# Optimization experiments

Measured on AMD Instinct MI355X. Metric: run time of the kernel, lower is better.

The kernel has to match this reference:

```python
import jax, jax.numpy as jnp
import numpy as np

B, S, D, H, E, K = 1, 2048, 1024, 16, 8, 2
DK = D // H          # 64 per-head key dim
FF = 4 * D           # 4096 expert hidden
EPS = 1e-5


def rmsnorm(x, scale):
    rms = jnp.sqrt(jnp.mean(x * x, axis=-1, keepdims=True) + EPS)
    return scale * (x / rms)


def setup_inputs() -> dict:
    key = jax.random.key(0)
    ks = jax.random.split(key, 12)
    std = 0.02
    x = jax.random.normal(ks[0], (B, S, D), dtype=jnp.float32)
    # causal mask: masked_fill where mask == 0
    self_attn_mask = jnp.tril(jnp.ones((S, S), dtype=jnp.int32))
    scale_attn = jnp.ones((D,), dtype=jnp.float32)
    scale_ffn = jnp.ones((D,), dtype=jnp.float32)
    # per-head projections, stacked: [H, DK, D] (torch Linear weight layout [out,in])
    Wq = jax.random.normal(ks[1], (H, DK, D), dtype=jnp.float32) * std
    Wk = jax.random.normal(ks[2], (H, DK, D), dtype=jnp.float32) * std
    Wv = jax.random.normal(ks[3], (H, DK, D), dtype=jnp.float32) * std
    Wo = jax.random.normal(ks[4], (D, D), dtype=jnp.float32) * std
    Wg = jax.random.normal(ks[5], (E, D), dtype=jnp.float32) * std   # router gate
    W_in = jax.random.normal(ks[6], (E, FF, D), dtype=jnp.float32) * std   # expert linear
    W_v = jax.random.normal(ks[7], (E, FF, D), dtype=jnp.float32) * std    # expert linear_v
    W_out = jax.random.normal(ks[8], (E, D, FF), dtype=jnp.float32) * std  # expert linear_out
    return {
        'x': x, 'self_attn_mask': self_attn_mask,
        'scale_attn': scale_attn, 'Wq': Wq, 'Wk': Wk, 'Wv': Wv, 'Wo': Wo,
        'scale_ffn': scale_ffn, 'Wg': Wg, 'W_in': W_in, 'W_v': W_v, 'W_out': W_out,
    }


def reference(x, self_attn_mask, scale_attn, Wq, Wk, Wv, Wo, scale_ffn, Wg, W_in, W_v, W_out):
    # --- self attention (pre-RMSNorm) ---
    normed = rmsnorm(x, scale_attn)
    q = jnp.einsum('bsd,hkd->bhsk', normed, Wq)
    k = jnp.einsum('bsd,hkd->bhsk', normed, Wk)
    v = jnp.einsum('bsd,hkd->bhsk', normed, Wv)
    attn = jnp.einsum('bhsk,bhtk->bhst', q, k) / np.sqrt(DK).astype(np.float32)
    attn = jnp.where(self_attn_mask[None, None] == 0, -jnp.inf, attn)
    attn = jax.nn.softmax(attn, axis=-1)
    ctx = jnp.einsum('bhst,bhtk->bhsk', attn, v)
    ctx = ctx.transpose(0, 2, 1, 3).reshape(x.shape[0], x.shape[1], D)  # concat heads
    a1 = ctx @ Wo.T
    x = x + a1
    # --- MoE (pre-RMSNorm) ---
    normed = rmsnorm(x, scale_ffn)
    router_logits = normed @ Wg.T                       # [B,S,E]
    router_probs = jax.nn.softmax(router_logits, axis=-1)
    gate, idx = jax.lax.top_k(router_probs, K)          # [B,S,K]
    gate = gate / jnp.sum(gate, axis=-1, keepdims=True)
    # combine weights per expert: sum of renormalized gates over selected slots
    onehot = (idx[..., None] == jnp.arange(E)).astype(x.dtype)  # [B,S,K,E]
    combine = jnp.sum(gate[..., None] * onehot, axis=2)         # [B,S,E]
    # all-expert dense FFN (faithful to the masked dense loop in torch)
    g = jax.nn.gelu(jnp.einsum('bsd,efd->bsef', normed, W_in), approximate=False)
    val = jnp.einsum('bsd,efd->bsef', normed, W_v)
    eo = jnp.einsum('bsef,edf->bsed', g * val, W_out)           # [B,S,E,D]
    moe_out = jnp.einsum('bse,bsed->bsd', combine, eo)
    out = x + moe_out
    return (out, router_probs)
```

## Files before the change

kernel.cpp:

```cpp
#include <hip/hip_runtime.h>
#include <hip/hip_bf16.h>
#include <math.h>

typedef unsigned int u32;
typedef unsigned short u16;
using bf16x8 = __attribute__((ext_vector_type(8))) short;
using f32x4 = __attribute__((ext_vector_type(4))) float;

#define MFMA_BF16(a, b, c) __builtin_amdgcn_mfma_f32_16x16x32_bf16((a), (b), (c), 0, 0, 0)
#define VMCNT8() asm volatile("s_waitcnt vmcnt(8)" ::: "memory")
#define VMCNT6() asm volatile("s_waitcnt vmcnt(6)" ::: "memory")
#define VMCNT4() asm volatile("s_waitcnt vmcnt(4)" ::: "memory")
#define VMCNT0() asm volatile("s_waitcnt vmcnt(0)" ::: "memory")
#define SBAR() __builtin_amdgcn_s_barrier()
#define SCHED0() __builtin_amdgcn_sched_barrier(0)

constexpr int kS = 2048, kD = 1024, kH = 16, kE = 8, kFF = 4096;
constexpr int kSlotCap = 5120;
constexpr int kMaxTiles = 40;
constexpr int kChunk = 8;

__device__ __forceinline__ u16 bf16_rne(float f) {
  u32 u = __float_as_uint(f);
  u32 r = (u + 0x7fffu + ((u >> 16) & 1u)) >> 16;
  return (u16)r;
}
__device__ __forceinline__ float bf16_f32(u16 h) { return __uint_as_float(((u32)h) << 16); }
__device__ __forceinline__ u32 pack_hl(float x) {
  u16 hi = bf16_rne(x);
  u16 lo = bf16_rne(x - bf16_f32(hi));
  return ((u32)lo << 16) | (u32)hi;
}
__device__ __forceinline__ void unpack8(const u32* t, bf16x8& h, bf16x8& l) {
#pragma unroll
  for (int j = 0; j < 8; j++) {
    h[j] = (short)(t[j] & 0xffffu);
    l[j] = (short)(t[j] >> 16);
  }
}
__device__ __forceinline__ void gload_lds16(const void* g, void* l) {
  __builtin_amdgcn_global_load_lds((const __attribute__((address_space(1))) u32*)g,
                                   (__attribute__((address_space(3))) u32*)l, 16, 0, 0);
}
__device__ __forceinline__ u32 cvtpk(float a, float b) {
  u32 r;
  asm("v_cvt_pk_bf16_f32 %0, %1, %2" : "=v"(r) : "v"(a), "v"(b));
  return r;
}

__global__ __launch_bounds__(256) void pack_dp3(const float* __restrict__ Wq,
                                                const float* __restrict__ Wk,
                                                const float* __restrict__ Wv,
                                                u16* __restrict__ o) {
  int i = blockIdx.x * 256 + threadIdx.x;
  if (i >= 3072 * 1024) return;
  int n = i >> 10, k = i & 1023;
  float v = (n < 1024) ? Wq[i] : (n < 2048) ? Wk[i - 1024 * 1024] : Wv[i - 2048 * 1024];
  u16 hi = bf16_rne(v);
  u16 lo = bf16_rne(v - bf16_f32(hi));
  size_t b = (size_t)n * 2048 + (size_t)(k >> 5) * 64 + (k & 31);
  o[b] = hi;
  o[b + 32] = lo;
}
__global__ __launch_bounds__(256) void pack_dp1(const float* __restrict__ W,
                                                u16* __restrict__ o, int n_elem) {
  int i = blockIdx.x * 256 + threadIdx.x;
  if (i >= n_elem) return;
  int k = i & 1023, n = i >> 10;
  float v = W[i];
  u16 hi = bf16_rne(v);
  u16 lo = bf16_rne(v - bf16_f32(hi));
  size_t b = (size_t)n * 2048 + (size_t)(k >> 5) * 64 + (k & 31);
  o[b] = hi;
  o[b + 32] = lo;
}
__global__ __launch_bounds__(256) void pack_bf16_kernel(const float* __restrict__ w,
                                                        u16* __restrict__ o, int n8) {
  int i = blockIdx.x * 256 + threadIdx.x;
  if (i >= n8) return;
  const float4* s = (const float4*)w + (size_t)i * 2;
  float4 a = s[0], b = s[1];
  u16 r[8] = {bf16_rne(a.x), bf16_rne(a.y), bf16_rne(a.z), bf16_rne(a.w),
              bf16_rne(b.x), bf16_rne(b.y), bf16_rne(b.z), bf16_rne(b.w)};
  *(uint4*)(o + (size_t)i * 8) = *(uint4*)r;
}

template <int MODE>
__global__ __launch_bounds__(256) void rmsnorm_kernel(
    const float* __restrict__ x, const float* __restrict__ scale,
    u16* __restrict__ odp, float* __restrict__ of32, u16* __restrict__ ob16) {
  const int s = blockIdx.x;
  const float* row = x + (size_t)s * kD;
  const int c = threadIdx.x * 4;
  float4 v = *(const float4*)(row + c);
  float ss = v.x * v.x + v.y * v.y + v.z * v.z + v.w * v.w;
#pragma unroll
  for (int m = 32; m; m >>= 1) ss += __shfl_xor(ss, m);
  __shared__ float wsum[4];
  if ((threadIdx.x & 63) == 0) wsum[threadIdx.x >> 6] = ss;
  __syncthreads();
  float tot = wsum[0] + wsum[1] + wsum[2] + wsum[3];
  float rinv = 1.0f / sqrtf(tot * (1.0f / kD) + 1e-5f);
  float4 sc = *(const float4*)(scale + c);
  float n[4] = {v.x * rinv * sc.x, v.y * rinv * sc.y, v.z * rinv * sc.z, v.w * rinv * sc.w};
  if (MODE == 0) {
    u16 hv[4], lv[4];
#pragma unroll
    for (int j = 0; j < 4; j++) {
      hv[j] = bf16_rne(n[j]);
      lv[j] = bf16_rne(n[j] - bf16_f32(hv[j]));
    }
    u16* o = odp + (size_t)s * 2048 + (size_t)(c >> 5) * 64 + (c & 31);
    *(uint2*)o = *(uint2*)hv;
    *(uint2*)(o + 32) = *(uint2*)lv;
  } else {
    *(float4*)(of32 + (size_t)s * kD + c) = make_float4(n[0], n[1], n[2], n[3]);
    u16* o = ob16 + (size_t)s * kD + c;
    o[0] = bf16_rne(n[0]); o[1] = bf16_rne(n[1]); o[2] = bf16_rne(n[2]); o[3] = bf16_rne(n[3]);
  }
}

template <int APK, int OUT>
__global__ __launch_bounds__(256) void gemm_dp(
    const void* __restrict__ Av, const u16* __restrict__ Bdp,
    const float* __restrict__ resid, int K,
    u32* __restrict__ oq, u32* __restrict__ ok, u32* __restrict__ ov,
    float* __restrict__ of) {
  __shared__ u16 As[2][128 * 64];
  __shared__ u16 Bs[2][128 * 64];
  const int tid = threadIdx.x, w = tid >> 6, l = tid & 63;
  const int m0 = blockIdx.y * 128, n0 = blockIdx.x * 128;
  const int wr = (w >> 1) * 64, wc = (w & 1) * 64;
  const char* Ab = (const char*)Av;
  const char* Bb = (const char*)Bdp;
  const size_t rowb = (size_t)K * 4;

  size_t asrc[4], bsrc[4];
  int dst[4];
#pragma unroll
  for (int i = 0; i < 4; i++) {
    int fl = i * 256 + tid;
    int row = fl >> 3, cb = fl & 7;
    size_t coff = (size_t)((cb ^ (row & 7)) * 16);
    asrc[i] = (size_t)(m0 + row) * rowb + coff;
    bsrc[i] = (size_t)(n0 + row) * rowb + coff;
    dst[i] = fl * 16;
  }

  f32x4 zero = {0.f, 0.f, 0.f, 0.f};
  f32x4 acc[4][4];
#pragma unroll
  for (int i = 0; i < 4; i++)
#pragma unroll
    for (int j = 0; j < 4; j++) acc[i][j] = zero;

  auto stage = [&](int buf, int s) {
    const char* ap = Ab + (size_t)s * 128;
    const char* bp = Bb + (size_t)s * 128;
#pragma unroll
    for (int i = 0; i < 4; i++) {
      gload_lds16(ap + asrc[i], (char*)&As[buf][0] + dst[i]);
      gload_lds16(bp + bsrc[i], (char*)&Bs[buf][0] + dst[i]);
    }
  };

  const int NS = K / 32;
  stage(0, 0);
  for (int s = 0; s < NS; s++) {
    const int cur = s & 1;
    const bool lastit = (s == NS - 1);
    if (!lastit) stage(cur ^ 1, s + 1);
    if (!lastit) VMCNT8(); else VMCNT0();
    SBAR();
    SCHED0();
    bf16x8 ah[4], al[4], bh[4], bl[4];
    const int g = l >> 4;
    if (APK) {
      const u32* At = (const u32*)&As[cur][0];
#pragma unroll
      for (int mi = 0; mi < 4; mi++) {
        int row = wr + mi * 16 + (l & 15);
        u32 t[8];
        *(uint4*)t = *(const uint4*)&At[row * 32 + (((2 * g) ^ (row & 7)) * 4)];
        *(uint4*)(t + 4) = *(const uint4*)&At[row * 32 + (((2 * g + 1) ^ (row & 7)) * 4)];
        unpack8(t, ah[mi], al[mi]);
      }
    } else {
#pragma unroll
      for (int mi = 0; mi < 4; mi++) {
        int row = wr + mi * 16 + (l & 15);
        ah[mi] = *(const bf16x8*)&As[cur][row * 64 + ((g ^ (row & 7)) * 8)];
        al[mi] = *(const bf16x8*)&As[cur][row * 64 + (((4 + g) ^ (row & 7)) * 8)];
      }
    }
#pragma unroll
    for (int ni = 0; ni < 4; ni++) {
      int row = wc + ni * 16 + (l & 15);
      bh[ni] = *(const bf16x8*)&Bs[cur][row * 64 + ((g ^ (row & 7)) * 8)];
      bl[ni] = *(const bf16x8*)&Bs[cur][row * 64 + (((4 + g) ^ (row & 7)) * 8)];
    }
#pragma unroll
    for (int mi = 0; mi < 4; mi++)
#pragma unroll
      for (int ni = 0; ni < 4; ni++) {
        f32x4 c = acc[mi][ni];
        c = MFMA_BF16(al[mi], bh[ni], c);
        c = MFMA_BF16(ah[mi], bl[ni], c);
        c = MFMA_BF16(ah[mi], bh[ni], c);
        acc[mi][ni] = c;
      }
    SCHED0();
    if (!lastit) SBAR();
  }

  if (OUT == 0) {
    u32* dstp;
    int nb;
    if (n0 < 1024) { dstp = oq; nb = n0; }
    else if (n0 < 2048) { dstp = ok; nb = n0 - 1024; }
    else { dstp = ov; nb = n0 - 2048; }
#pragma unroll
    for (int mi = 0; mi < 4; mi++)
#pragma unroll
      for (int ni = 0; ni < 4; ni++)
#pragma unroll
        for (int r = 0; r < 4; r++) {
          int row = m0 + wr + mi * 16 + ((l >> 4) << 2) + r;
          int col = nb + wc + ni * 16 + (l & 15);
          dstp[(size_t)row * 1024 + col] = pack_hl(acc[mi][ni][r]);
        }
  } else {
#pragma unroll
    for (int mi = 0; mi < 4; mi++)
#pragma unroll
      for (int ni = 0; ni < 4; ni++)
#pragma unroll
        for (int r = 0; r < 4; r++) {
          int row = m0 + wr + mi * 16 + ((l >> 4) << 2) + r;
          int col = n0 + wc + ni * 16 + (l & 15);
          of[(size_t)row * 1024 + col] = resid[(size_t)row * 1024 + col] + acc[mi][ni][r];
        }
  }
}

__global__ __launch_bounds__(256) void attn_kernel(
    const u32* __restrict__ Qp, const u32* __restrict__ Kp, const u32* __restrict__ Vp,
    float* __restrict__ Opart, float* __restrict__ mpart, float* __restrict__ lpart) {
  constexpr int LDK = 68;
  __shared__ u32 Ks[64 * LDK];
  __shared__ u32 Vs[64 * LDK];
  __shared__ u32 Ps[64 * LDK];
  const int tid = threadIdx.x, w = tid >> 6, l = tid & 63;
  int b = blockIdx.x, qt, c;
  if (b < 8) { qt = b; c = 0; }
  else if (b < 24) { qt = 8 + ((b - 8) >> 1); c = (b - 8) & 1; }
  else if (b < 48) { qt = 16 + (b - 24) / 3; c = (b - 24) % 3; }
  else { qt = 24 + ((b - 48) >> 2); c = (b - 48) & 3; }
  const int hh = blockIdx.y;
  const int q0 = qt * 64, hc = hh * 64;
  const int kt0 = c * kChunk;
  const int kt1 = min(kt0 + kChunk, qt + 1);

  bf16x8 qh[2], ql[2];
  {
    const int qrow = q0 + w * 16 + (l & 15);
#pragma unroll
    for (int kk = 0; kk < 2; kk++) {
      u32 t[8];
      const u32* p = Qp + (size_t)qrow * kD + hc + kk * 32 + ((l >> 4) << 3);
      *(uint4*)t = *(const uint4*)p;
      *(uint4*)(t + 4) = *(const uint4*)(p + 4);
      unpack8(t, qh[kk], ql[kk]);
    }
  }
  float mrun[4], lrun[4];
  f32x4 zero = {0.f, 0.f, 0.f, 0.f};
  f32x4 oacc[4];
#pragma unroll
  for (int r = 0; r < 4; r++) { mrun[r] = -3.0e38f; lrun[r] = 0.f; }
#pragma unroll
  for (int vb = 0; vb < 4; vb++) oacc[vb] = zero;

  const int trow = tid >> 2, c0v = (tid & 3) * 16;
  const u32* gKb = Kp + hc + c0v;
  const u32* gVb = Vp + hc + c0v;
  uint4 kr[4], vr[4];
  {
    const u32* gK = gKb + (size_t)(kt0 * 64 + trow) * kD;
    kr[0] = *(const uint4*)gK; kr[1] = *(const uint4*)(gK + 4);
    kr[2] = *(const uint4*)(gK + 8); kr[3] = *(const uint4*)(gK + 12);
    const u32* gV = gVb + (size_t)(kt0 * 64 + trow) * kD;
    vr[0] = *(const uint4*)gV; vr[1] = *(const uint4*)(gV + 4);
    vr[2] = *(const uint4*)(gV + 8); vr[3] = *(const uint4*)(gV + 12);
  }

  for (int kt = kt0; kt < kt1; kt++) {
    {
      u32* sK = Ks + trow * LDK + c0v;
      *(uint4*)sK = kr[0]; *(uint4*)(sK + 4) = kr[1];
      *(uint4*)(sK + 8) = kr[2]; *(uint4*)(sK + 12) = kr[3];
#pragma unroll
      for (int j = 0; j < 4; j++) {
        Vs[(c0v + j * 4 + 0) * LDK + trow] = vr[j].x;
        Vs[(c0v + j * 4 + 1) * LDK + trow] = vr[j].y;
        Vs[(c0v + j * 4 + 2) * LDK + trow] = vr[j].z;
        Vs[(c0v + j * 4 + 3) * LDK + trow] = vr[j].w;
      }
    }
    __syncthreads();
    if (kt + 1 < kt1) {
      const u32* gK = gKb + (size_t)((kt + 1) * 64 + trow) * kD;
      kr[0] = *(const uint4*)gK; kr[1] = *(const uint4*)(gK + 4);
      kr[2] = *(const uint4*)(gK + 8); kr[3] = *(const uint4*)(gK + 12);
      const u32* gV = gVb + (size_t)((kt + 1) * 64 + trow) * kD;
      vr[0] = *(const uint4*)gV; vr[1] = *(const uint4*)(gV + 4);
      vr[2] = *(const uint4*)(gV + 8); vr[3] = *(const uint4*)(gV + 12);
    }

    f32x4 sfr[4];
#pragma unroll
    for (int kb = 0; kb < 4; kb++) {
      f32x4 sa = zero;
#pragma unroll
      for (int kk = 0; kk < 2; kk++) {
        u32 t[8];
        bf16x8 kh, kl;
        const u32* p = Ks + (kb * 16 + (l & 15)) * LDK + kk * 32 + ((l >> 4) << 3);
        *(uint4*)t = *(const uint4*)p;
        *(uint4*)(t + 4) = *(const uint4*)(p + 4);
        unpack8(t, kh, kl);
        sa = MFMA_BF16(ql[kk], kl, sa);
        sa = MFMA_BF16(ql[kk], kh, sa);
        sa = MFMA_BF16(qh[kk], kl, sa);
        sa = MFMA_BF16(qh[kk], kh, sa);
      }
      sfr[kb] = sa * 0.125f;
    }
    if (kt == qt) {
#pragma unroll
      for (int kb = 0; kb < 4; kb++) {
        int t = kt * 64 + kb * 16 + (l & 15);
#pragma unroll
        for (int r = 0; r < 4; r++) {
          int qq = q0 + w * 16 + ((l >> 4) << 2) + r;
          if (t > qq) sfr[kb][r] = -3.0e38f;
        }
      }
    }
#pragma unroll
    for (int r = 0; r < 4; r++) {
      float mx = fmaxf(fmaxf(sfr[0][r], sfr[1][r]), fmaxf(sfr[2][r], sfr[3][r]));
#pragma unroll
      for (int mm = 1; mm < 16; mm <<= 1) mx = fmaxf(mx, __shfl_xor(mx, mm));
      float mnew = fmaxf(mrun[r], mx);
      float sf = __expf(mrun[r] - mnew);
      mrun[r] = mnew;
      float rs = 0.f;
#pragma unroll
      for (int kb = 0; kb < 4; kb++) {
        float p = __expf(sfr[kb][r] - mnew);
        sfr[kb][r] = p;
        rs += p;
      }
#pragma unroll
      for (int mm = 1; mm < 16; mm <<= 1) rs += __shfl_xor(rs, mm);
      lrun[r] = lrun[r] * sf + rs;
#pragma unroll
      for (int vb = 0; vb < 4; vb++) oacc[vb][r] *= sf;
    }
#pragma unroll
    for (int kb = 0; kb < 4; kb++)
#pragma unroll
      for (int r = 0; r < 4; r++)
        Ps[(w * 16 + ((l >> 4) << 2) + r) * LDK + kb * 16 + (l & 15)] = pack_hl(sfr[kb][r]);
#pragma unroll
    for (int ks = 0; ks < 2; ks++) {
      bf16x8 ph, pl;
      {
        u32 t[8];
        const u32* pp = Ps + (w * 16 + (l & 15)) * LDK + ks * 32 + ((l >> 4) << 3);
        *(uint4*)t = *(const uint4*)pp;
        *(uint4*)(t + 4) = *(const uint4*)(pp + 4);
        unpack8(t, ph, pl);
      }
#pragma unroll
      for (int vb = 0; vb < 4; vb++) {
        u32 t2[8];
        bf16x8 vh, vl;
        const u32* pv = Vs + (vb * 16 + (l & 15)) * LDK + ks * 32 + ((l >> 4) << 3);
        *(uint4*)t2 = *(const uint4*)pv;
        *(uint4*)(t2 + 4) = *(const uint4*)(pv + 4);
        unpack8(t2, vh, vl);
        f32x4 cc = oacc[vb];
        cc = MFMA_BF16(pl, vl, cc);
        cc = MFMA_BF16(pl, vh, cc);
        cc = MFMA_BF16(ph, vl, cc);
        cc = MFMA_BF16(ph, vh, cc);
        oacc[vb] = cc;
      }
    }
    __syncthreads();
  }

  const int p = (qt * 16 + hh) * 4 + c;
  float* Po = Opart + (size_t)p * 4096;
#pragma unroll
  for (int vb = 0; vb < 4; vb++)
#pragma unroll
    for (int r = 0; r < 4; r++) {
      int rl = w * 16 + ((l >> 4) << 2) + r;
      int cl = vb * 16 + (l & 15);
      Po[rl * 64 + cl] = oacc[vb][r];
    }
  if ((l & 15) == 0) {
#pragma unroll
    for (int r = 0; r < 4; r++) {
      int rl = w * 16 + ((l >> 4) << 2) + r;
      mpart[p * 64 + rl] = mrun[r];
      lpart[p * 64 + rl] = lrun[r];
    }
  }
}

__global__ __launch_bounds__(256) void attn_merge(
    const float* __restrict__ Opart, const float* __restrict__ mpart,
    const float* __restrict__ lpart, u32* __restrict__ Op) {
  const int qt = blockIdx.x, hh = blockIdx.y;
  const int nch = (qt + kChunk) >> 3;
  const int t = threadIdx.x;
  const int row = t >> 2;
  const int c0 = (t & 3) * 16;
  const int pbase = (qt * 16 + hh) * 4;
  float M = -3.0e38f;
  for (int c = 0; c < nch; c++) M = fmaxf(M, mpart[(pbase + c) * 64 + row]);
  float den = 0.f;
  float acc[16];
#pragma unroll
  for (int j = 0; j < 16; j++) acc[j] = 0.f;
  for (int c = 0; c < nch; c++) {
    float wgt = __expf(mpart[(pbase + c) * 64 + row] - M);
    den += wgt * lpart[(pbase + c) * 64 + row];
    const float* po = Opart + (size_t)(pbase + c) * 4096 + row * 64 + c0;
#pragma unroll
    for (int j = 0; j < 16; j += 4) {
      float4 v = *(const float4*)(po + j);
      acc[j] += wgt * v.x; acc[j + 1] += wgt * v.y;
      acc[j + 2] += wgt * v.z; acc[j + 3] += wgt * v.w;
    }
  }
  float inv = 1.f / den;
  u32* dst = Op + (size_t)(qt * 64 + row) * kD + hh * 64 + c0;
#pragma unroll
  for (int j = 0; j < 16; j++) dst[j] = pack_hl(acc[j] * inv);
}

__global__ __launch_bounds__(256) void router_kernel(
    const float* __restrict__ normed, const float* __restrict__ Wg,
    float* __restrict__ probs, float* __restrict__ gates,
    int* __restrict__ experts, int* __restrict__ counts) {
  const int w = threadIdx.x >> 6, l = threadIdx.x & 63;
  const int s = blockIdx.x * 4 + w;
  float lg[kE];
  const float* row = normed + (size_t)s * kD;
#pragma unroll
  for (int e = 0; e < kE; e++) {
    const float* wg = Wg + (size_t)e * kD;
    float a = 0.f;
    for (int d = l; d < kD; d += 64) a += row[d] * wg[d];
#pragma unroll
    for (int m = 32; m; m >>= 1) a += __shfl_xor(a, m);
    lg[e] = a;
  }
  if (l == 0) {
    float mx = lg[0];
#pragma unroll
    for (int e = 1; e < kE; e++) mx = fmaxf(mx, lg[e]);
    float p[kE], sum = 0.f;
#pragma unroll
    for (int e = 0; e < kE; e++) { p[e] = __expf(lg[e] - mx); sum += p[e]; }
    float inv = 1.f / sum;
#pragma unroll
    for (int e = 0; e < kE; e++) { p[e] *= inv; probs[(size_t)s * kE + e] = p[e]; }
    int i1 = 0;
#pragma unroll
    for (int e = 1; e < kE; e++) if (lg[e] > lg[i1]) i1 = e;
    int i2 = (i1 == 0) ? 1 : 0;
#pragma unroll
    for (int e = 0; e < kE; e++) if (e != i1 && lg[e] > lg[i2]) i2 = e;
    float den = 1.f / (p[i1] + p[i2]);
    gates[s * 2] = p[i1] * den;
    gates[s * 2 + 1] = p[i2] * den;
    experts[s * 2] = i1;
    experts[s * 2 + 1] = i2;
    atomicAdd(&counts[i1], 1);
    atomicAdd(&counts[i2], 1);
  }
}

__global__ void moe_init(int* counts) {
  if (threadIdx.x < kE) counts[threadIdx.x] = 0;
}
__global__ void moe_scan(const int* __restrict__ counts, int* __restrict__ ebase,
                         int* __restrict__ cursor, int2* __restrict__ tmap) {
  if (threadIdx.x == 0) {
    int acc = 0, t = 0;
    for (int e = 0; e < kE; e++) {
      ebase[e] = acc;
      cursor[e] = acc;
      int nt = (counts[e] + 127) >> 7;
      for (int i = 0; i < nt; i++) tmap[t++] = make_int2(e, i * 128);
      acc += nt << 7;
    }
    ebase[kE] = acc;
    for (; t < kMaxTiles; t++) tmap[t] = make_int2(-1, 0);
  }
}
__global__ void moe_fill(const int* __restrict__ experts, int* __restrict__ cursor,
                         int* __restrict__ slot_list, int* __restrict__ slot_of) {
  int s = blockIdx.x * 256 + threadIdx.x;
  if (s >= kS) return;
  for (int k = 0; k < 2; k++) {
    int e = experts[s * 2 + k];
    int pos = atomicAdd(&cursor[e], 1);
    slot_list[pos] = s;
    slot_of[s * 2 + k] = pos;
  }
}

__global__ __launch_bounds__(256) void moe_mmA(
    const u16* __restrict__ A, const float* __restrict__ Wi, const float* __restrict__ Wv2,
    const int* __restrict__ slot_list, const int* __restrict__ counts,
    const int* __restrict__ ebase, const int2* __restrict__ tmap,
    u16* __restrict__ H) {
  int2 tm = tmap[blockIdx.y];
  const int e = tm.x;
  if (e < 0) return;
  const int base = ebase[e], Me = counts[e], m0 = tm.y;
  const int n0 = blockIdx.x * 128;
  __shared__ u16 As[2][64 * 64];
  __shared__ float Bsf[2][128 * 32];
  const int tid = threadIdx.x, w = tid >> 6, l = tid & 63;
  const int wr = (w >> 1) * 64, wc = (w & 1) * 64;
  const char* Ab = (const char*)A;

  size_t asrc[2];
  int adst[2];
#pragma unroll
  for (int i = 0; i < 2; i++) {
    int fl = i * 256 + tid;
    int lrow = fl >> 3, sl = fl & 7;
    int sp = sl ^ (lrow & 7);
    int t = 2 * lrow + (sp >> 2);
    int cbl = sp & 3;
    int mr = m0 + t;
    if (mr > Me - 1) mr = Me - 1;
    int ar = slot_list[base + mr];
    asrc[i] = (size_t)ar * 2048 + (size_t)cbl * 16;
    adst[i] = fl * 16;
  }
  const char* bptr[4];
  int bdst[4];
#pragma unroll
  for (int i = 0; i < 4; i++) {
    int fl = i * 256 + tid;
    int row = fl >> 3, sl = fl & 7;
    int sp = sl ^ (row & 7);
    int nn = n0 + row;
    const float* srcT = (nn & 1) ? Wv2 : Wi;
    bptr[i] = (const char*)(srcT + ((size_t)e * 4096 + (nn >> 1)) * 1024) + sp * 16;
    bdst[i] = fl * 16;
  }

  const int g = l >> 4;
  int aoff[4], boff0[4], boff1[4];
#pragma unroll
  for (int mi = 0; mi < 4; mi++) {
    int t = wr + mi * 16 + (l & 15);
    int lr = t >> 1;
    int sl = (((t & 1) << 2) | g) ^ (lr & 7);
    aoff[mi] = lr * 128 + sl * 16;
  }
#pragma unroll
  for (int ni = 0; ni < 4; ni++) {
    int rr = wc + ni * 16 + (l & 15);
    boff0[ni] = rr * 128 + (((2 * g) ^ (rr & 7)) * 16);
    boff1[ni] = rr * 128 + (((2 * g + 1) ^ (rr & 7)) * 16);
  }

  f32x4 zero = {0.f, 0.f, 0.f, 0.f};
  f32x4 acc[4][4];
#pragma unroll
  for (int i = 0; i < 4; i++)
#pragma unroll
    for (int j = 0; j < 4; j++) acc[i][j] = zero;

  auto stage = [&](int buf, int s) {
    const size_t soA = (size_t)s * 64;
    const size_t soB = (size_t)s * 128;
#pragma unroll
    for (int i = 0; i < 2; i++)
      gload_lds16(Ab + soA + asrc[i], (char*)&As[buf][0] + adst[i]);
#pragma unroll
    for (int i = 0; i < 4; i++)
      gload_lds16(bptr[i] + soB, (char*)&Bsf[buf][0] + bdst[i]);
  };

  const int NS = kD / 32;
  stage(0, 0);
  for (int s = 0; s < NS; s++) {
    const int cur = s & 1;
    const bool lastit = (s == NS - 1);
    if (!lastit) stage(cur ^ 1, s + 1);
    if (!lastit) VMCNT6(); else VMCNT0();
    SBAR();
    SCHED0();
    const char* Ac = (const char*)&As[cur][0];
    const char* Bc = (const char*)&Bsf[cur][0];
    bf16x8 af[4], bfr[4];
#pragma unroll
    for (int mi = 0; mi < 4; mi++) af[mi] = *(const bf16x8*)(Ac + aoff[mi]);
#pragma unroll
    for (int ni = 0; ni < 4; ni++) {
      float4 f0 = *(const float4*)(Bc + boff0[ni]);
      float4 f1 = *(const float4*)(Bc + boff1[ni]);
      u32 pk[4];
      pk[0] = cvtpk(f0.x, f0.y);
      pk[1] = cvtpk(f0.z, f0.w);
      pk[2] = cvtpk(f1.x, f1.y);
      pk[3] = cvtpk(f1.z, f1.w);
      bfr[ni] = *(bf16x8*)pk;
    }
#pragma unroll
    for (int mi = 0; mi < 4; mi++)
#pragma unroll
      for (int ni = 0; ni < 4; ni++) acc[mi][ni] = MFMA_BF16(af[mi], bfr[ni], acc[mi][ni]);
    SCHED0();
    if (!lastit) SBAR();
  }

#pragma unroll
  for (int mi = 0; mi < 4; mi++)
#pragma unroll
    for (int r = 0; r < 4; r++) {
      int ml = m0 + wr + mi * 16 + ((l >> 4) << 2) + r;
      if (ml >= Me) continue;
      size_t rb = (size_t)(base + ml) * 4096;
#pragma unroll
      for (int ni = 0; ni < 4; ni++) {
        int col = n0 + wc + ni * 16 + (l & 15);
        float v0 = acc[mi][ni][r];
        float pv = __shfl_xor(v0, 1);
        if ((l & 1) == 0) {
          float ge = 0.5f * v0 * (1.0f + erff(v0 * 0.70710678118654752f));
          H[rb + (col >> 1)] = bf16_rne(ge * pv);
        }
      }
    }
}

__global__ __launch_bounds__(256) void moe_mm2(
    const u16* __restrict__ H, const u16* __restrict__ Bg,
    const int* __restrict__ counts, const int* __restrict__ ebase,
    const int2* __restrict__ tmap, float* __restrict__ eo) {
  int2 tm = tmap[blockIdx.y];
  const int e = tm.x;
  if (e < 0) return;
  const int base = ebase[e], Me = counts[e], m0 = tm.y;
  const int n0 = blockIdx.x * 64;
  __shared__ u16 As[2][128 * 64];
  __shared__ u16 Bs[2][64 * 64];
  const int tid = threadIdx.x, w = tid >> 6, l = tid & 63;
  const int wr = (w >> 1) * 64, wc = (w & 1) * 32;
  const char* Ab = (const char*)H;
  const char* Bb = (const char*)(Bg + (size_t)e * kD * kFF);

  size_t asrc[4], bsrc[2];
  int adst[4], bdst[2];
#pragma unroll
  for (int i = 0; i < 4; i++) {
    int fl = i * 256 + tid;
    int row = fl >> 3, cb = fl & 7;
    int mr = m0 + row;
    if (mr > Me - 1) mr = Me - 1;
    asrc[i] = (size_t)(base + mr) * 8192 + (size_t)((cb ^ (row & 7)) * 16);
    adst[i] = fl * 16;
  }
#pragma unroll
  for (int i = 0; i < 2; i++) {
    int fl = i * 256 + tid;
    int row = fl >> 3, cb = fl & 7;
    bsrc[i] = (size_t)(n0 + row) * 8192 + (size_t)((cb ^ (row & 7)) * 16);
    bdst[i] = fl * 16;
  }

  f32x4 zero = {0.f, 0.f, 0.f, 0.f};
  f32x4 acc[4][2];
#pragma unroll
  for (int i = 0; i < 4; i++)
#pragma unroll
    for (int j = 0; j < 2; j++) acc[i][j] = zero;

  auto stage = [&](int buf, int s) {
    const size_t so = (size_t)s * 128;
#pragma unroll
    for (int i = 0; i < 4; i++) gload_lds16(Ab + so + asrc[i], (char*)&As[buf][0] + adst[i]);
#pragma unroll
    for (int i = 0; i < 2; i++) gload_lds16(Bb + so + bsrc[i], (char*)&Bs[buf][0] + bdst[i]);
  };

  const int NS = kFF / 64;
  stage(0, 0);
  for (int s = 0; s < NS; s++) {
    const int cur = s & 1;
    const bool lastit = (s == NS - 1);
    if (!lastit) stage(cur ^ 1, s + 1);
    if (!lastit) VMCNT6(); else VMCNT0();
    SBAR();
    SCHED0();
#pragma unroll
    for (int kk = 0; kk < 2; kk++) {
      const int g = kk * 4 + (l >> 4);
      bf16x8 af[4], bfr[2];
#pragma unroll
      for (int mi = 0; mi < 4; mi++) {
        int row = wr + mi * 16 + (l & 15);
        af[mi] = *(const bf16x8*)&As[cur][row * 64 + ((g ^ (row & 7)) * 8)];
      }
#pragma unroll
      for (int ni = 0; ni < 2; ni++) {
        int row = wc + ni * 16 + (l & 15);
        bfr[ni] = *(const bf16x8*)&Bs[cur][row * 64 + ((g ^ (row & 7)) * 8)];
      }
#pragma unroll
      for (int mi = 0; mi < 4; mi++)
#pragma unroll
        for (int ni = 0; ni < 2; ni++) acc[mi][ni] = MFMA_BF16(af[mi], bfr[ni], acc[mi][ni]);
    }
    SCHED0();
    if (!lastit) SBAR();
  }

#pragma unroll
  for (int mi = 0; mi < 4; mi++)
#pragma unroll
    for (int r = 0; r < 4; r++) {
      int ml = m0 + wr + mi * 16 + ((l >> 4) << 2) + r;
      if (ml >= Me) continue;
      size_t rb = (size_t)(base + ml) * kD;
#pragma unroll
      for (int ni = 0; ni < 2; ni++) {
        int col = n0 + wc + ni * 16 + (l & 15);
        eo[rb + col] = acc[mi][ni][r];
      }
    }
}

__global__ __launch_bounds__(256) void combine_kernel(
    const float* __restrict__ h, const float* __restrict__ eo,
    const float* __restrict__ gates, const int* __restrict__ slot_of,
    float* __restrict__ out) {
  const int s = blockIdx.x;
  const float g0 = gates[s * 2], g1 = gates[s * 2 + 1];
  const int p0 = slot_of[s * 2], p1 = slot_of[s * 2 + 1];
  const int c = threadIdx.x * 4;
  float4 hv = *(const float4*)(h + (size_t)s * kD + c);
  float4 e0 = *(const float4*)(eo + (size_t)p0 * kD + c);
  float4 e1 = *(const float4*)(eo + (size_t)p1 * kD + c);
  float4 o;
  o.x = hv.x + g0 * e0.x + g1 * e1.x;
  o.y = hv.y + g0 * e0.y + g1 * e1.y;
  o.z = hv.z + g0 * e0.z + g1 * e1.z;
  o.w = hv.w + g0 * e0.w + g1 * e1.w;
  *(float4*)(out + (size_t)s * kD + c) = o;
}

extern "C" void kernel_launch(void* const* d_in, const int* in_sizes, int n_in,
                              void* d_out, int out_size, void* d_ws, size_t ws_size,
                              hipStream_t stream) {
  (void)in_sizes; (void)n_in; (void)out_size; (void)ws_size;
  const float* x = (const float*)d_in[0];
  const float* scale_attn = (const float*)d_in[2];
  const float* Wq = (const float*)d_in[3];
  const float* Wk = (const float*)d_in[4];
  const float* Wv = (const float*)d_in[5];
  const float* Wo = (const float*)d_in[6];
  const float* scale_ffn = (const float*)d_in[7];
  const float* Wg = (const float*)d_in[8];
  const float* W_in = (const float*)d_in[9];
  const float* W_vv = (const float*)d_in[10];
  const float* W_out = (const float*)d_in[11];
  float* out = (float*)d_out;
  float* probs = out + (size_t)kS * kD;

  char* wsb = (char*)d_ws;
  size_t off = 0;
  auto alloc = [&](size_t bytes) -> void* {
    void* p = wsb + off;
    off += (bytes + 255) & ~(size_t)255;
    return p;
  };
  const size_t SDu = (size_t)kS * kD;
  u16* normA_dp = (u16*)alloc(SDu * 4);
  u32* qpk = (u32*)alloc(SDu * 4);
  u32* kpk = (u32*)alloc(SDu * 4);
  u32* vpk = (u32*)alloc(SDu * 4);
  u32* ctxpk = (u32*)alloc(SDu * 4);
  u16* Wqkv_dp = (u16*)alloc((size_t)3072 * 2048 * 2);
  u16* Wo_dp = (u16*)alloc((size_t)1024 * 2048 * 2);
  float* normFf = (float*)alloc(SDu * 4);
  float* eo = (float*)alloc((size_t)kSlotCap * kD * 4);
  float* h = (float*)alloc(SDu * 4);
  u16* normFb = (u16*)alloc(SDu * 2);
  u16* Wout_bf = (u16*)alloc((size_t)kE * kD * kFF * 2);
  u16* H = (u16*)alloc((size_t)kSlotCap * kFF * 2);
  float* Opart = (float*)alloc((size_t)2048 * 4096 * 4);
  float* mpart = (float*)alloc((size_t)2048 * 64 * 4);
  float* lpart = (float*)alloc((size_t)2048 * 64 * 4);
  float* gates = (float*)alloc(kS * 2 * 4);
  int* experts = (int*)alloc(kS * 2 * 4);
  int* slot_of = (int*)alloc(kS * 2 * 4);
  int* slot_list = (int*)alloc(kSlotCap * 4);
  int* counts = (int*)alloc(64);
  int* ebase = (int*)alloc(64);
  int* cursor = (int*)alloc(64);
  int2* tmap = (int2*)alloc(kMaxTiles * 8);

  pack_dp3<<<(3072 * 1024) / 256, 256, 0, stream>>>(Wq, Wk, Wv, Wqkv_dp);
  pack_dp1<<<(1024 * 1024) / 256, 256, 0, stream>>>(Wo, Wo_dp, 1024 * 1024);
  const int n8o = (int)((size_t)kE * kD * kFF / 8);
  pack_bf16_kernel<<<(n8o + 255) / 256, 256, 0, stream>>>(W_out, Wout_bf, n8o);

  rmsnorm_kernel<0><<<kS, 256, 0, stream>>>(x, scale_attn, normA_dp, nullptr, nullptr);
  gemm_dp<0, 0><<<dim3(3072 / 128, kS / 128), 256, 0, stream>>>(
      normA_dp, Wqkv_dp, nullptr, kD, qpk, kpk, vpk, nullptr);
  attn_kernel<<<dim3(80, kH), 256, 0, stream>>>(qpk, kpk, vpk, Opart, mpart, lpart);
  attn_merge<<<dim3(kS / 64, kH), 256, 0, stream>>>(Opart, mpart, lpart, ctxpk);
  gemm_dp<1, 1><<<dim3(1024 / 128, kS / 128), 256, 0, stream>>>(
      ctxpk, Wo_dp, x, kD, nullptr, nullptr, nullptr, h);

  rmsnorm_kernel<1><<<kS, 256, 0, stream>>>(h, scale_ffn, nullptr, normFf, normFb);
  moe_init<<<1, 64, 0, stream>>>(counts);
  router_kernel<<<kS / 4, 256, 0, stream>>>(normFf, Wg, probs, gates, experts, counts);
  moe_scan<<<1, 64, 0, stream>>>(counts, ebase, cursor, tmap);
  moe_fill<<<kS / 256, 256, 0, stream>>>(experts, cursor, slot_list, slot_of);

  moe_mmA<<<dim3(8192 / 128, kMaxTiles), 256, 0, stream>>>(
      normFb, W_in, W_vv, slot_list, counts, ebase, tmap, H);
  moe_mm2<<<dim3(kD / 64, kMaxTiles), 256, 0, stream>>>(
      H, Wout_bf, counts, ebase, tmap, eo);

  combine_kernel<<<kS, 256, 0, stream>>>(h, eo, gates, slot_of, out);
}
```

Before: 626.9 us.

## Fuse W_out bf16 conversion into moe_mm2 by loading fp32 weights directly

Drops the separate pack pass that converts the full expert output weight (8x1024x4096 fp32) to bf16. moe_mm2 now streams the fp32 W_out tiles into LDS and converts them to bf16 in registers before the MFMA. K-steps shrink from 64 to 32, which doubles the iteration count and adds conversion work per tile. The intent is to save the standalone pass that reads 128MB and writes 64MB. The cost is that each tile reloads fp32 weights, twice the bytes of bf16, for every row tile that reuses them.

```diff
diff --git a/kernel.cpp b/kernel.cpp
--- a/kernel.cpp
+++ b/kernel.cpp
@@ -73,16 +73,6 @@
   size_t b = (size_t)n * 2048 + (size_t)(k >> 5) * 64 + (k & 31);
   o[b] = hi;
   o[b + 32] = lo;
-}
-__global__ __launch_bounds__(256) void pack_bf16_kernel(const float* __restrict__ w,
-                                                        u16* __restrict__ o, int n8) {
-  int i = blockIdx.x * 256 + threadIdx.x;
-  if (i >= n8) return;
-  const float4* s = (const float4*)w + (size_t)i * 2;
-  float4 a = s[0], b = s[1];
-  u16 r[8] = {bf16_rne(a.x), bf16_rne(a.y), bf16_rne(a.z), bf16_rne(a.w),
-              bf16_rne(b.x), bf16_rne(b.y), bf16_rne(b.z), bf16_rne(b.w)};
-  *(uint4*)(o + (size_t)i * 8) = *(uint4*)r;
 }
 
 template <int MODE>
@@ -659,7 +649,7 @@
 }
 
 __global__ __launch_bounds__(256) void moe_mm2(
-    const u16* __restrict__ H, const u16* __restrict__ Bg,
+    const u16* __restrict__ H, const float* __restrict__ Wo_f,
     const int* __restrict__ counts, const int* __restrict__ ebase,
     const int2* __restrict__ tmap, float* __restrict__ eo) {
   int2 tm = tmap[blockIdx.y];
@@ -667,30 +657,51 @@
   if (e < 0) return;
   const int base = ebase[e], Me = counts[e], m0 = tm.y;
   const int n0 = blockIdx.x * 64;
-  __shared__ u16 As[2][128 * 64];
-  __shared__ u16 Bs[2][64 * 64];
+  __shared__ u16 As[2][64 * 64];
+  __shared__ float Bsf[2][64 * 32];
   const int tid = threadIdx.x, w = tid >> 6, l = tid & 63;
   const int wr = (w >> 1) * 64, wc = (w & 1) * 32;
   const char* Ab = (const char*)H;
-  const char* Bb = (const char*)(Bg + (size_t)e * kD * kFF);
-
-  size_t asrc[4], bsrc[2];
-  int adst[4], bdst[2];
-#pragma unroll
-  for (int i = 0; i < 4; i++) {
-    int fl = i * 256 + tid;
-    int row = fl >> 3, cb = fl & 7;
-    int mr = m0 + row;
-    if (mr > Me - 1) mr = Me - 1;
-    asrc[i] = (size_t)(base + mr) * 8192 + (size_t)((cb ^ (row & 7)) * 16);
-    adst[i] = fl * 16;
-  }
+
+  size_t asrc[2];
+  int adst[2];
 #pragma unroll
   for (int i = 0; i < 2; i++) {
     int fl = i * 256 + tid;
-    int row = fl >> 3, cb = fl & 7;
-    bsrc[i] = (size_t)(n0 + row) * 8192 + (size_t)((cb ^ (row & 7)) * 16);
+    int lrow = fl >> 3, sl = fl & 7;
+    int sp = sl ^ (lrow & 7);
+    int t = 2 * lrow + (sp >> 2);
+    int cbl = sp & 3;
+    int mr = m0 + t;
+    if (mr > Me - 1) mr = Me - 1;
+    asrc[i] = (size_t)(base + mr) * 8192 + (size_t)cbl * 16;
+    adst[i] = fl * 16;
+  }
+  const char* bptr[2];
+  int bdst[2];
+#pragma unroll
+  for (int i = 0; i < 2; i++) {
+    int fl = i * 256 + tid;
+    int row = fl >> 3, sl = fl & 7;
+    int sp = sl ^ (row & 7);
+    bptr[i] = (const char*)(Wo_f + ((size_t)e * 1024 + n0 + row) * 4096) + sp * 16;
     bdst[i] = fl * 16;
+  }
+
+  const int g = l >> 4;
+  int aoff[4], boff0[2], boff1[2];
+#pragma unroll
+  for (int mi = 0; mi < 4; mi++) {
+    int t = wr + mi * 16 + (l & 15);
+    int lr = t >> 1;
+    int sl = (((t & 1) << 2) | g) ^ (lr & 7);
+    aoff[mi] = lr * 128 + sl * 16;
+  }
+#pragma unroll
+  for (int ni = 0; ni < 2; ni++) {
+    int rr = wc + ni * 16 + (l & 15);
+    boff0[ni] = rr * 128 + (((2 * g) ^ (rr & 7)) * 16);
+    boff1[ni] = rr * 128 + (((2 * g + 1) ^ (rr & 7)) * 16);
   }
 
   f32x4 zero = {0.f, 0.f, 0.f, 0.f};
@@ -701,41 +712,45 @@
     for (int j = 0; j < 2; j++) acc[i][j] = zero;
 
   auto stage = [&](int buf, int s) {
-    const size_t so = (size_t)s * 128;
-#pragma unroll
-    for (int i = 0; i < 4; i++) gload_lds16(Ab + so + asrc[i], (char*)&As[buf][0] + adst[i]);
-#pragma unroll
-    for (int i = 0; i < 2; i++) gload_lds16(Bb + so + bsrc[i], (char*)&Bs[buf][0] + bdst[i]);
+    const size_t soA = (size_t)s * 64;
+    const size_t soB = (size_t)s * 128;
+#pragma unroll
+    for (int i = 0; i < 2; i++)
+      gload_lds16(Ab + soA + asrc[i], (char*)&As[buf][0] + adst[i]);
+#pragma unroll
+    for (int i = 0; i < 2; i++)
+      gload_lds16(bptr[i] + soB, (char*)&Bsf[buf][0] + bdst[i]);
   };
 
-  const int NS = kFF / 64;
+  const int NS = kFF / 32;
   stage(0, 0);
   for (int s = 0; s < NS; s++) {
     const int cur = s & 1;
     const bool lastit = (s == NS - 1);
     if (!lastit) stage(cur ^ 1, s + 1);
-    if (!lastit) VMCNT6(); else VMCNT0();
+    if (!lastit) VMCNT4(); else VMCNT0();
     SBAR();
     SCHED0();
-#pragma unroll
-    for (int kk = 0; kk < 2; kk++) {
-      const int g = kk * 4 + (l >> 4);
-      bf16x8 af[4], bfr[2];
-#pragma unroll
-      for (int mi = 0; mi < 4; mi++) {
-        int row = wr + mi * 16 + (l & 15);
-        af[mi] = *(const bf16x8*)&As[cur][row * 64 + ((g ^ (row & 7)) * 8)];
-      }
-#pragma unroll
-      for (int ni = 0; ni < 2; ni++) {
-        int row = wc + ni * 16 + (l & 15);
-        bfr[ni] = *(const bf16x8*)&Bs[cur][row * 64 + ((g ^ (row & 7)) * 8)];
-      }
-#pragma unroll
-      for (int mi = 0; mi < 4; mi++)
-#pragma unroll
-        for (int ni = 0; ni < 2; ni++) acc[mi][ni] = MFMA_BF16(af[mi], bfr[ni], acc[mi][ni]);
-    }
+    const char* Ac = (const char*)&As[cur][0];
+    const char* Bc = (const char*)&Bsf[cur][0];
+    bf16x8 af[4], bfr[2];
+#pragma unroll
+    for (int mi = 0; mi < 4; mi++) af[mi] = *(const bf16x8*)(Ac + aoff[mi]);
+#pragma unroll
+    for (int ni = 0; ni < 2; ni++) {
+      float4 f0 = *(const float4*)(Bc + boff0[ni]);
+      float4 f1 = *(const float4*)(Bc + boff1[ni]);
+      u32 pk[4];
+      pk[0] = cvtpk(f0.x, f0.y);
+      pk[1] = cvtpk(f0.z, f0.w);
+      pk[2] = cvtpk(f1.x, f1.y);
+      pk[3] = cvtpk(f1.z, f1.w);
+      bfr[ni] = *(bf16x8*)pk;
+    }
+#pragma unroll
+    for (int mi = 0; mi < 4; mi++)
+#pragma unroll
+      for (int ni = 0; ni < 2; ni++) acc[mi][ni] = MFMA_BF16(af[mi], bfr[ni], acc[mi][ni]);
     SCHED0();
     if (!lastit) SBAR();
   }
@@ -811,7 +826,6 @@
   float* eo = (float*)alloc((size_t)kSlotCap * kD * 4);
   float* h = (float*)alloc(SDu * 4);
   u16* normFb = (u16*)alloc(SDu * 2);
-  u16* Wout_bf = (u16*)alloc((size_t)kE * kD * kFF * 2);
   u16* H = (u16*)alloc((size_t)kSlotCap * kFF * 2);
   float* Opart = (float*)alloc((size_t)2048 * 4096 * 4);
   float* mpart = (float*)alloc((size_t)2048 * 64 * 4);
@@ -827,8 +841,6 @@
 
   pack_dp3<<<(3072 * 1024) / 256, 256, 0, stream>>>(Wq, Wk, Wv, Wqkv_dp);
   pack_dp1<<<(1024 * 1024) / 256, 256, 0, stream>>>(Wo, Wo_dp, 1024 * 1024);
-  const int n8o = (int)((size_t)kE * kD * kFF / 8);
-  pack_bf16_kernel<<<(n8o + 255) / 256, 256, 0, stream>>>(W_out, Wout_bf, n8o);
 
   rmsnorm_kernel<0><<<kS, 256, 0, stream>>>(x, scale_attn, normA_dp, nullptr, nullptr);
   gemm_dp<0, 0><<<dim3(3072 / 128, kS / 128), 256, 0, stream>>>(
@@ -847,7 +859,7 @@
   moe_mmA<<<dim3(8192 / 128, kMaxTiles), 256, 0, stream>>>(
       normFb, W_in, W_vv, slot_list, counts, ebase, tmap, H);
   moe_mm2<<<dim3(kD / 64, kMaxTiles), 256, 0, stream>>>(
-      H, Wout_bf, counts, ebase, tmap, eo);
+      H, W_out, counts, ebase, tmap, eo);
 
   combine_kernel<<<kS, 256, 0, stream>>>(h, eo, gates, slot_of, out);
 }
```

New measurement: 625.1 us, median of 2. About the same (-0.3%).
